# Optimization experiments

Measured on AMD Instinct MI355X. Metric: run time of the kernel, lower is better.

## Reference

```python
import jax, jax.numpy as jnp
import numpy as np

NUM_HEADS = 16
HEAD_DIM = 64
HIDDEN = NUM_HEADS * HEAD_DIM  # 1024
B, S = 4, 2048
SCALE = HEAD_DIM ** -0.5


def setup_inputs() -> dict:
    key = jax.random.key(0)
    ks = jax.random.split(key, 5)
    hidden_states = jax.random.normal(ks[0], (B, S, HIDDEN), dtype=jnp.float32)
    # additive causal mask: 0 on/below diagonal, -1e9 above
    causal = jnp.tril(jnp.ones((S, S), dtype=bool))
    attention_mask = jnp.where(causal, 0.0, -1e9).astype(jnp.float32)[None, None]  # [1,1,S,S]
    init = 1.0 / np.sqrt(HIDDEN)
    wq = jax.random.normal(ks[1], (HIDDEN, HIDDEN), dtype=jnp.float32) * init
    wk = jax.random.normal(ks[2], (HIDDEN, HIDDEN), dtype=jnp.float32) * init
    wv = jax.random.normal(ks[3], (HIDDEN, HIDDEN), dtype=jnp.float32) * init
    wo = jax.random.normal(ks[4], (HIDDEN, HIDDEN), dtype=jnp.float32) * init
    return {"hidden_states": hidden_states, "attention_mask": attention_mask,
            "wq": wq, "wk": wk, "wv": wv, "wo": wo}


def reference(hidden_states, attention_mask, wq, wk, wv, wo):
    b, s, _ = hidden_states.shape
    # nn.Linear(bias=False): y = x @ W^T ; split heads -> [b, h, s, d]
    def proj(w):
        return (hidden_states @ w.T).reshape(b, s, NUM_HEADS, HEAD_DIM).transpose(0, 2, 1, 3)
    q, k, v = proj(wq), proj(wk), proj(wv)
    scores = jnp.einsum('bhqd,bhkd->bhqk', q, k) * SCALE  # [b,h,s,s] materialized
    scores = scores + attention_mask
    probs = jax.nn.softmax(scores, axis=-1)  # dropout is identity (eval / p=0)
    attn = jnp.einsum('bhqk,bhkd->bhqd', probs, v)
    attn = attn.transpose(0, 2, 1, 3).reshape(b, s, HIDDEN)
    return attn @ wo.T
```

## Files before the change

### kernel.cpp

```cpp
#include <hip/hip_runtime.h>

typedef unsigned short u16;
typedef __attribute__((ext_vector_type(8))) short bf16x8;
typedef __attribute__((ext_vector_type(4))) float f32x4;
typedef __attribute__((ext_vector_type(16))) float f32x16;
typedef __attribute__((ext_vector_type(2))) __bf16 bf16x2;

#define NUMH 16
#define HD   64
#define HID  1024
#define BB   4
#define SS   2048
#define MM   (BB*SS)

__device__ __forceinline__ u16 f2bf(float f){
  unsigned u = __builtin_bit_cast(unsigned, f);
  u += 0x7FFFu + ((u >> 16) & 1u);
  return (u16)(u >> 16);
}

__device__ __forceinline__ unsigned pack_bf16(float a, float b){
  bf16x2 t; t[0] = (__bf16)a; t[1] = (__bf16)b;
  return __builtin_bit_cast(unsigned, t);
}

__device__ __forceinline__ float exp2_fast(float x){
  float r; asm("v_exp_f32 %0, %1" : "=v"(r) : "v"(x)); return r;
}

__device__ __forceinline__ void gload_lds16(const void* g, void* l){
  __builtin_amdgcn_global_load_lds((const __attribute__((address_space(1))) void*)g,
                                   (__attribute__((address_space(3))) void*)l, 16, 0, 0);
}

__global__ __launch_bounds__(256) void cast_all(const float* __restrict__ hs,
    const float* __restrict__ wq, const float* __restrict__ wk,
    const float* __restrict__ wv, const float* __restrict__ wo,
    u16* __restrict__ dst)
{
  const int NX4 = MM*HID/4;
  const int NW4 = HID*HID/4;
  int i = blockIdx.x * 256 + threadIdx.x;
  const float* src; int local;
  if (i < NX4){ src = hs; local = i; }
  else {
    int j = i - NX4;
    int wsel = j >> 18;
    local = j & (NW4 - 1);
    src = (wsel == 0) ? wq : ((wsel == 1) ? wk : ((wsel == 2) ? wv : wo));
  }
  float4 v = reinterpret_cast<const float4*>(src)[local];
  ushort4 o = make_ushort4(f2bf(v.x), f2bf(v.y), f2bf(v.z), f2bf(v.w));
  reinterpret_cast<ushort4*>(dst)[i] = o;
}

__global__ __launch_bounds__(256) void gemm_qkv(const u16* __restrict__ A,
    const u16* __restrict__ Wq, const u16* __restrict__ Wk, const u16* __restrict__ Wv,
    u16* __restrict__ Qo, u16* __restrict__ Ko, u16* __restrict__ Vto)
{
  __shared__ alignas(16) u16 As[128*64];
  __shared__ alignas(16) u16 Bs[128*64];
  const int tid = threadIdx.x;
  const int w = tid >> 6, l = tid & 63;
  const int wr = w >> 1, wc = w & 1;
  const int lr = l & 15, lg = l >> 4;
  const int bm = blockIdx.x, bn = blockIdx.y;
  const int which = bn >> 3;
  const int ncol0 = (bn & 7) * 128;
  const u16* __restrict__ Bmat = (which == 0) ? Wq : ((which == 1) ? Wk : Wv);
  const int row0 = bm * 128;

  f32x4 acc[4][4];
  #pragma unroll
  for (int i = 0; i < 4; ++i)
    #pragma unroll
    for (int j = 0; j < 4; ++j)
      acc[i][j] = (f32x4){0.f, 0.f, 0.f, 0.f};

  const int srow = l >> 3;
  const int cg8  = ((l & 7) ^ srow) * 8;

  for (int kt = 0; kt < HID/64; ++kt){
    __syncthreads();
    #pragma unroll
    for (int j = 0; j < 4; ++j){
      int rr = j*32 + w*8 + srow;
      gload_lds16(A    + (size_t)(row0  + rr)*HID + kt*64 + cg8, (char*)As + j*4096 + w*1024);
      gload_lds16(Bmat + (size_t)(ncol0 + rr)*HID + kt*64 + cg8, (char*)Bs + j*4096 + w*1024);
    }
    __syncthreads();
    #pragma unroll
    for (int kk = 0; kk < 2; ++kk){
      bf16x8 af[4], bfr[4];
      #pragma unroll
      for (int i = 0; i < 4; ++i){
        const int offb = ((kk*4 + lg) ^ (lr & 7)) * 16;
        af[i]  = *(const bf16x8*)((const char*)As + (wr*64 + i*16 + lr)*128 + offb);
        bfr[i] = *(const bf16x8*)((const char*)Bs + (wc*64 + i*16 + lr)*128 + offb);
      }
      if (which == 2){
        #pragma unroll
        for (int i = 0; i < 4; ++i)
          #pragma unroll
          for (int j = 0; j < 4; ++j)
            acc[i][j] = __builtin_amdgcn_mfma_f32_16x16x32_bf16(bfr[j], af[i], acc[i][j], 0, 0, 0);
      } else {
        #pragma unroll
        for (int i = 0; i < 4; ++i)
          #pragma unroll
          for (int j = 0; j < 4; ++j)
            acc[i][j] = __builtin_amdgcn_mfma_f32_16x16x32_bf16(af[i], bfr[j], acc[i][j], 0, 0, 0);
      }
    }
  }

  if (which == 2){
    #pragma unroll
    for (int i = 0; i < 4; ++i){
      #pragma unroll
      for (int j = 0; j < 4; ++j){
        #pragma unroll
        for (int r = 0; r < 4; ++r){
          int nl = ncol0 + wc*64 + j*16 + lg*4 + r;
          int gm = row0 + wr*64 + i*16 + lr;
          int b_ = gm >> 11, s = gm & 2047;
          int h  = nl >> 6,  d = nl & 63;
          Vto[(((size_t)b_*NUMH + h)*HD + d)*SS + s] = f2bf(acc[i][j][r]);
        }
      }
    }
  } else {
    #pragma unroll
    for (int i = 0; i < 4; ++i){
      #pragma unroll
      for (int j = 0; j < 4; ++j){
        #pragma unroll
        for (int r = 0; r < 4; ++r){
          int gm = row0 + wr*64 + i*16 + lg*4 + r;
          int nl = ncol0 + wc*64 + j*16 + lr;
          int b_ = gm >> 11, s = gm & 2047;
          int h  = nl >> 6,  d = nl & 63;
          float v = acc[i][j][r];
          if (which == 0)
            Qo[(((size_t)b_*NUMH + h)*SS + s)*HD + d] = f2bf(v * 0.18033688f);
          else
            Ko[(((size_t)b_*NUMH + h)*SS + s)*HD + d] = f2bf(v);
        }
      }
    }
  }
}

__global__ __launch_bounds__(256) void gemm_out(const u16* __restrict__ A,
    const u16* __restrict__ Wo, float* __restrict__ C)
{
  __shared__ alignas(16) u16 As[128*64];
  __shared__ alignas(16) u16 Bs[128*64];
  const int tid = threadIdx.x;
  const int w = tid >> 6, l = tid & 63;
  const int wr = w >> 1, wc = w & 1;
  const int lr = l & 15, lg = l >> 4;
  const int row0 = blockIdx.x * 128;
  const int ncol0 = blockIdx.y * 128;

  f32x4 acc[4][4];
  #pragma unroll
  for (int i = 0; i < 4; ++i)
    #pragma unroll
    for (int j = 0; j < 4; ++j)
      acc[i][j] = (f32x4){0.f, 0.f, 0.f, 0.f};

  const int srow = l >> 3;
  const int cg8  = ((l & 7) ^ srow) * 8;

  for (int kt = 0; kt < HID/64; ++kt){
    __syncthreads();
    #pragma unroll
    for (int j = 0; j < 4; ++j){
      int rr = j*32 + w*8 + srow;
      gload_lds16(A  + (size_t)(row0  + rr)*HID + kt*64 + cg8, (char*)As + j*4096 + w*1024);
      gload_lds16(Wo + (size_t)(ncol0 + rr)*HID + kt*64 + cg8, (char*)Bs + j*4096 + w*1024);
    }
    __syncthreads();
    #pragma unroll
    for (int kk = 0; kk < 2; ++kk){
      bf16x8 af[4], bfr[4];
      #pragma unroll
      for (int i = 0; i < 4; ++i){
        const int offb = ((kk*4 + lg) ^ (lr & 7)) * 16;
        af[i]  = *(const bf16x8*)((const char*)As + (wr*64 + i*16 + lr)*128 + offb);
        bfr[i] = *(const bf16x8*)((const char*)Bs + (wc*64 + i*16 + lr)*128 + offb);
      }
      #pragma unroll
      for (int i = 0; i < 4; ++i)
        #pragma unroll
        for (int j = 0; j < 4; ++j)
          acc[i][j] = __builtin_amdgcn_mfma_f32_16x16x32_bf16(af[i], bfr[j], acc[i][j], 0, 0, 0);
    }
  }

  #pragma unroll
  for (int i = 0; i < 4; ++i)
    #pragma unroll
    for (int j = 0; j < 4; ++j)
      #pragma unroll
      for (int r = 0; r < 4; ++r){
        int gm = row0 + wr*64 + i*16 + lg*4 + r;
        int nl = ncol0 + wc*64 + j*16 + lr;
        C[(size_t)gm*HID + nl] = acc[i][j][r];
      }
}

__device__ __forceinline__ void stage_kv(const u16* __restrict__ Kg, const u16* __restrict__ Vt,
    size_t bhB, int kv0, u16* Kbuf, u16* Vbuf, int w, int l)
{
  #pragma unroll
  for (int i = 0; i < 2; ++i){
    const int r = 32*i + 8*w + (l >> 3);
    const int c16 = (l & 7) ^ (r & 7);
    gload_lds16(Kg + bhB + (size_t)(kv0 + r)*HD + c16*8, (char*)Kbuf + i*4096 + w*1024);
    gload_lds16(Vt + bhB + (size_t)r*SS + kv0 + c16*8,   (char*)Vbuf + i*4096 + w*1024);
  }
}

__global__ __launch_bounds__(256) void attn_fwd(const u16* __restrict__ Qg,
    const u16* __restrict__ Kg, const u16* __restrict__ Vt, u16* __restrict__ AO)
{
  __shared__ alignas(16) u16 Ks[2][64*64];
  __shared__ alignas(16) u16 Vs[2][64*64];

  const int tid = threadIdx.x;
  const int w = tid >> 6, l = tid & 63;
  const int lq = l & 31, hi = l >> 5;
  const int wgid = blockIdx.x;
  const int bh = (wgid & 7) + 8*((wgid >> 3) & 7);
  const int strip = 15 - (wgid >> 6);
  const int b_ = bh >> 4, h = bh & 15;
  const size_t bhB = (size_t)bh * SS * HD;

  const int qs0 = strip * 128;
  const int nt = 2*strip + 2;
  const int q0w = qs0 + 32*w;
  const int qabs = q0w + lq;

  bf16x8 qf[4];
  #pragma unroll
  for (int c = 0; c < 4; ++c)
    qf[c] = *(const bf16x8*)(Qg + bhB + (size_t)qabs*HD + c*16 + hi*8);

  float lsum = 0.f;
  f32x16 oacc[2];
  #pragma unroll
  for (int n = 0; n < 2; ++n)
    #pragma unroll
    for (int r = 0; r < 16; ++r) oacc[n][r] = 0.f;

  int cur = 0;
  stage_kv(Kg, Vt, bhB, 0, Ks[0], Vs[0], w, l);
  __syncthreads();

  for (int t = 0; t < nt; ++t){
    const int kv0 = t*64;
    if (t + 1 < nt)
      stage_kv(Kg, Vt, bhB, (t+1)*64, Ks[cur^1], Vs[cur^1], w, l);

    if (kv0 <= q0w + 31){
      const u16* Kb = Ks[cur];
      const u16* Vb = Vs[cur];
      f32x16 sacc[2];
      #pragma unroll
      for (int mi = 0; mi < 2; ++mi)
        #pragma unroll
        for (int r = 0; r < 16; ++r) sacc[mi][r] = 0.f;
      __builtin_amdgcn_s_setprio(1);
      #pragma unroll
      for (int mi = 0; mi < 2; ++mi){
        const int krow = mi*32 + lq;
        const int sw = (krow & 7) << 4;
        #pragma unroll
        for (int c = 0; c < 4; ++c){
          bf16x8 kf = *(const bf16x8*)((const char*)Kb + krow*128 + ((c*32 + hi*16) ^ sw));
          sacc[mi] = __builtin_amdgcn_mfma_f32_32x32x16_bf16(kf, qf[c], sacc[mi], 0, 0, 0);
        }
      }
      __builtin_amdgcn_s_setprio(0);
      if (kv0 + 63 > q0w){
        #pragma unroll
        for (int mi = 0; mi < 2; ++mi)
          #pragma unroll
          for (int r = 0; r < 16; ++r){
            int kabs = kv0 + mi*32 + (r & 3) + 8*(r >> 2) + 4*hi;
            if (kabs > qabs) sacc[mi][r] = -1e30f;
          }
      }
      float ps[4] = {0.f, 0.f, 0.f, 0.f};
      #pragma unroll
      for (int mi = 0; mi < 2; ++mi)
        #pragma unroll
        for (int r = 0; r < 16; ++r){
          float p = exp2_fast(sacc[mi][r]);
          sacc[mi][r] = p;
          ps[r & 3] += p;
        }
      float psum = (ps[0] + ps[1]) + (ps[2] + ps[3]);
      psum += __shfl_xor(psum, 32);
      lsum += psum;

      bf16x8 pf[4];
      #pragma unroll
      for (int c = 0; c < 4; ++c){
        const int mi = c >> 1;
        const int geb = (c & 1) * 8;
        unsigned a0 = pack_bf16(sacc[mi][geb+0], sacc[mi][geb+1]);
        unsigned a1 = pack_bf16(sacc[mi][geb+2], sacc[mi][geb+3]);
        unsigned b0 = pack_bf16(sacc[mi][geb+4], sacc[mi][geb+5]);
        unsigned b1 = pack_bf16(sacc[mi][geb+6], sacc[mi][geb+7]);
        unsigned sel0 = hi ? b0 : a0, sel1 = hi ? b1 : a1;
        unsigned oth0 = hi ? a0 : b0, oth1 = hi ? a1 : b1;
        unsigned rcv0 = (unsigned)__shfl_xor((int)oth0, 32);
        unsigned rcv1 = (unsigned)__shfl_xor((int)oth1, 32);
        union { unsigned u[4]; bf16x8 v; } pu;
        pu.u[0] = hi ? rcv0 : sel0;
        pu.u[1] = hi ? rcv1 : sel1;
        pu.u[2] = hi ? sel0 : rcv0;
        pu.u[3] = hi ? sel1 : rcv1;
        pf[c] = pu.v;
      }

      __builtin_amdgcn_s_setprio(1);
      #pragma unroll
      for (int n = 0; n < 2; ++n){
        const int drow = n*32 + lq;
        const int swv = (drow & 7) << 4;
        #pragma unroll
        for (int c = 0; c < 4; ++c){
          bf16x8 vf = *(const bf16x8*)((const char*)Vb + drow*128 + ((c*32 + hi*16) ^ swv));
          oacc[n] = __builtin_amdgcn_mfma_f32_32x32x16_bf16(vf, pf[c], oacc[n], 0, 0, 0);
        }
      }
      __builtin_amdgcn_s_setprio(0);
    }
    __syncthreads();
    cur ^= 1;
  }

  const float inv = 1.f / lsum;
  u16* dst = AO + ((size_t)b_*SS + qabs)*HID + h*HD;
  #pragma unroll
  for (int n = 0; n < 2; ++n)
    #pragma unroll
    for (int g = 0; g < 4; ++g){
      ushort4 o;
      o.x = f2bf(oacc[n][4*g+0] * inv);
      o.y = f2bf(oacc[n][4*g+1] * inv);
      o.z = f2bf(oacc[n][4*g+2] * inv);
      o.w = f2bf(oacc[n][4*g+3] * inv);
      *(ushort4*)(dst + n*32 + 8*g + 4*hi) = o;
    }
}

extern "C" void kernel_launch(void* const* d_in, const int* in_sizes, int n_in,
                              void* d_out, int out_size, void* d_ws, size_t ws_size,
                              hipStream_t stream)
{
  const float* hs = (const float*)d_in[0];
  const float* wq = (const float*)d_in[2];
  const float* wk = (const float*)d_in[3];
  const float* wv = (const float*)d_in[4];
  const float* wo = (const float*)d_in[5];

  char* ws = (char*)d_ws;
  u16* Xb  = (u16*)(ws);
  u16* Wqb = (u16*)(ws + ((size_t)16 << 20));
  u16* Wkb = (u16*)(ws + ((size_t)18 << 20));
  u16* Wvb = (u16*)(ws + ((size_t)20 << 20));
  u16* Wob = (u16*)(ws + ((size_t)22 << 20));
  u16* Q   = (u16*)(ws + ((size_t)24 << 20));
  u16* Kb  = (u16*)(ws + ((size_t)40 << 20));
  u16* Vt  = (u16*)(ws + ((size_t)56 << 20));
  u16* AO  = (u16*)(ws + ((size_t)72 << 20));

  cast_all<<<12288, 256, 0, stream>>>(hs, wq, wk, wv, wo, Xb);

  gemm_qkv<<<dim3(64, 24), 256, 0, stream>>>(Xb, Wqb, Wkb, Wvb, Q, Kb, Vt);
  attn_fwd<<<1024, 256, 0, stream>>>(Q, Kb, Vt, AO);
  gemm_out<<<dim3(64, 8), 256, 0, stream>>>(AO, Wob, (float*)d_out);
}
```

Baseline: 154.7 us.

## Triple-buffer QKV GEMM with 256x128 tiles and interleaved async loads

Rewrites the QKV projection GEMM to use 512-thread blocks computing 256x128 tiles, with a three-stage LDS ring in dynamic shared memory (147 KB). Global-to-LDS loads for tile t+2 are issued in pieces between MFMA sub-steps, with explicit vmcnt waits, barriers and setprio around the MFMA clusters. The aim is to hide global load latency and raise arithmetic intensity per block. In exchange it uses far more LDS, halves the grid to 768 blocks, and relies on hand-tuned waitcnt counts that must match the issued loads exactly.

```diff
diff --git a/kernel.cpp b/kernel.cpp
--- a/kernel.cpp
+++ b/kernel.cpp
@@ -54,75 +54,120 @@
   reinterpret_cast<ushort4*>(dst)[i] = o;
 }
 
-__global__ __launch_bounds__(256) void gemm_qkv(const u16* __restrict__ A,
+__global__ __launch_bounds__(512, 2) void gemm_qkv(const u16* __restrict__ A,
     const u16* __restrict__ Wq, const u16* __restrict__ Wk, const u16* __restrict__ Wv,
     u16* __restrict__ Qo, u16* __restrict__ Ko, u16* __restrict__ Vto)
 {
-  __shared__ alignas(16) u16 As[128*64];
-  __shared__ alignas(16) u16 Bs[128*64];
+  extern __shared__ char smem[];
   const int tid = threadIdx.x;
   const int w = tid >> 6, l = tid & 63;
-  const int wr = w >> 1, wc = w & 1;
+  const int wm = w >> 2, wn = w & 3;
   const int lr = l & 15, lg = l >> 4;
   const int bm = blockIdx.x, bn = blockIdx.y;
   const int which = bn >> 3;
   const int ncol0 = (bn & 7) * 128;
   const u16* __restrict__ Bmat = (which == 0) ? Wq : ((which == 1) ? Wk : Wv);
-  const int row0 = bm * 128;
-
-  f32x4 acc[4][4];
-  #pragma unroll
-  for (int i = 0; i < 4; ++i)
-    #pragma unroll
-    for (int j = 0; j < 4; ++j)
-      acc[i][j] = (f32x4){0.f, 0.f, 0.f, 0.f};
-
-  const int srow = l >> 3;
-  const int cg8  = ((l & 7) ^ srow) * 8;
-
-  for (int kt = 0; kt < HID/64; ++kt){
-    __syncthreads();
-    #pragma unroll
-    for (int j = 0; j < 4; ++j){
-      int rr = j*32 + w*8 + srow;
-      gload_lds16(A    + (size_t)(row0  + rr)*HID + kt*64 + cg8, (char*)As + j*4096 + w*1024);
-      gload_lds16(Bmat + (size_t)(ncol0 + rr)*HID + kt*64 + cg8, (char*)Bs + j*4096 + w*1024);
-    }
-    __syncthreads();
-    #pragma unroll
-    for (int kk = 0; kk < 2; ++kk){
-      bf16x8 af[4], bfr[4];
-      #pragma unroll
-      for (int i = 0; i < 4; ++i){
-        const int offb = ((kk*4 + lg) ^ (lr & 7)) * 16;
-        af[i]  = *(const bf16x8*)((const char*)As + (wr*64 + i*16 + lr)*128 + offb);
-        bfr[i] = *(const bf16x8*)((const char*)Bs + (wc*64 + i*16 + lr)*128 + offb);
-      }
+  const int row0 = bm * 256;
+
+  const int sr  = l >> 3;
+  const int cg8 = ((l & 7) ^ sr) * 8;
+  const int dstw = w * 1024;
+
+  auto stageA2 = [&](int kt, int c, int u0){
+    char* base = smem + c * 49152;
+    #pragma unroll
+    for (int u = u0; u < u0 + 2; ++u)
+      gload_lds16(A + (size_t)(row0 + u*64 + w*8 + sr)*HID + kt*64 + cg8,
+                  base + u*8192 + dstw);
+  };
+  auto stageB2 = [&](int kt, int c){
+    char* base = smem + c * 49152 + 32768;
+    #pragma unroll
+    for (int u = 0; u < 2; ++u)
+      gload_lds16(Bmat + (size_t)(ncol0 + u*64 + w*8 + sr)*HID + kt*64 + cg8,
+                  base + u*8192 + dstw);
+  };
+
+  f32x4 acc[8][2] = {};
+
+  stageA2(0, 0, 0); stageA2(0, 0, 2); stageB2(0, 0);
+  stageA2(1, 1, 0); stageA2(1, 1, 2); stageB2(1, 1);
+  asm volatile("s_waitcnt vmcnt(6)" ::: "memory");
+  __builtin_amdgcn_s_barrier();
+  asm volatile("" ::: "memory");
+
+  int c = 0;
+  for (int t = 0; t < 16; ++t){
+    const char* Ab = smem + c * 49152;
+    const char* Bb = Ab + 32768;
+    int c2 = c + 2; if (c2 >= 3) c2 -= 3;
+    const bool pre = (t < 14);
+    bf16x8 bfr[2][2];
+    #pragma unroll
+    for (int p = 0; p < 4; ++p){
+      bf16x8 af[2][2];
+      #pragma unroll
+      for (int i2 = 0; i2 < 2; ++i2){
+        const int row = wm*128 + (2*p + i2)*16 + lr;
+        #pragma unroll
+        for (int kk = 0; kk < 2; ++kk)
+          af[i2][kk] = *(const bf16x8*)(Ab + row*128 + ((kk*4 + lg) ^ (lr & 7))*16);
+      }
+      if (p == 0){
+        #pragma unroll
+        for (int j = 0; j < 2; ++j){
+          const int rowb = wn*32 + j*16 + lr;
+          #pragma unroll
+          for (int kk = 0; kk < 2; ++kk)
+            bfr[j][kk] = *(const bf16x8*)(Bb + rowb*128 + ((kk*4 + lg) ^ (lr & 7))*16);
+        }
+      }
+      if (pre){
+        if (p == 0) stageA2(t+2, c2, 0);
+        else if (p == 1) stageA2(t+2, c2, 2);
+        else if (p == 2) stageB2(t+2, c2);
+      }
+      __builtin_amdgcn_s_barrier();
+      asm volatile("s_waitcnt lgkmcnt(0)" ::: "memory");
+      __builtin_amdgcn_sched_barrier(0);
+      __builtin_amdgcn_s_setprio(1);
       if (which == 2){
         #pragma unroll
-        for (int i = 0; i < 4; ++i)
+        for (int i2 = 0; i2 < 2; ++i2)
           #pragma unroll
-          for (int j = 0; j < 4; ++j)
-            acc[i][j] = __builtin_amdgcn_mfma_f32_16x16x32_bf16(bfr[j], af[i], acc[i][j], 0, 0, 0);
+          for (int j = 0; j < 2; ++j)
+            #pragma unroll
+            for (int kk = 0; kk < 2; ++kk)
+              acc[2*p+i2][j] = __builtin_amdgcn_mfma_f32_16x16x32_bf16(bfr[j][kk], af[i2][kk], acc[2*p+i2][j], 0, 0, 0);
       } else {
         #pragma unroll
-        for (int i = 0; i < 4; ++i)
+        for (int i2 = 0; i2 < 2; ++i2)
           #pragma unroll
-          for (int j = 0; j < 4; ++j)
-            acc[i][j] = __builtin_amdgcn_mfma_f32_16x16x32_bf16(af[i], bfr[j], acc[i][j], 0, 0, 0);
-      }
-    }
+          for (int j = 0; j < 2; ++j)
+            #pragma unroll
+            for (int kk = 0; kk < 2; ++kk)
+              acc[2*p+i2][j] = __builtin_amdgcn_mfma_f32_16x16x32_bf16(af[i2][kk], bfr[j][kk], acc[2*p+i2][j], 0, 0, 0);
+      }
+      __builtin_amdgcn_s_setprio(0);
+      if (p == 3){
+        if (t < 14)       asm volatile("s_waitcnt vmcnt(6)" ::: "memory");
+        else if (t == 14) asm volatile("s_waitcnt vmcnt(0)" ::: "memory");
+      }
+      __builtin_amdgcn_s_barrier();
+      asm volatile("" ::: "memory");
+    }
+    c += 1; if (c == 3) c = 0;
   }
 
   if (which == 2){
     #pragma unroll
-    for (int i = 0; i < 4; ++i){
-      #pragma unroll
-      for (int j = 0; j < 4; ++j){
+    for (int i = 0; i < 8; ++i){
+      #pragma unroll
+      for (int j = 0; j < 2; ++j){
         #pragma unroll
         for (int r = 0; r < 4; ++r){
-          int nl = ncol0 + wc*64 + j*16 + lg*4 + r;
-          int gm = row0 + wr*64 + i*16 + lr;
+          int nl = ncol0 + wn*32 + j*16 + lg*4 + r;
+          int gm = row0 + wm*128 + i*16 + lr;
           int b_ = gm >> 11, s = gm & 2047;
           int h  = nl >> 6,  d = nl & 63;
           Vto[(((size_t)b_*NUMH + h)*HD + d)*SS + s] = f2bf(acc[i][j][r]);
@@ -131,13 +176,13 @@
     }
   } else {
     #pragma unroll
-    for (int i = 0; i < 4; ++i){
-      #pragma unroll
-      for (int j = 0; j < 4; ++j){
+    for (int i = 0; i < 8; ++i){
+      #pragma unroll
+      for (int j = 0; j < 2; ++j){
         #pragma unroll
         for (int r = 0; r < 4; ++r){
-          int gm = row0 + wr*64 + i*16 + lg*4 + r;
-          int nl = ncol0 + wc*64 + j*16 + lr;
+          int gm = row0 + wm*128 + i*16 + lg*4 + r;
+          int nl = ncol0 + wn*32 + j*16 + lr;
           int b_ = gm >> 11, s = gm & 2047;
           int h  = nl >> 6,  d = nl & 63;
           float v = acc[i][j][r];
@@ -380,9 +425,16 @@
   u16* Vt  = (u16*)(ws + ((size_t)56 << 20));
   u16* AO  = (u16*)(ws + ((size_t)72 << 20));
 
+  static int attr_set = 0;
+  if (!attr_set){
+    hipFuncSetAttribute((const void*)gemm_qkv,
+                        hipFuncAttributeMaxDynamicSharedMemorySize, 147456);
+    attr_set = 1;
+  }
+
   cast_all<<<12288, 256, 0, stream>>>(hs, wq, wk, wv, wo, Xb);
 
-  gemm_qkv<<<dim3(64, 24), 256, 0, stream>>>(Xb, Wqb, Wkb, Wvb, Q, Kb, Vt);
+  gemm_qkv<<<dim3(32, 24), 512, 147456, stream>>>(Xb, Wqb, Wkb, Wvb, Q, Kb, Vt);
   attn_fwd<<<1024, 256, 0, stream>>>(Q, Kb, Vt, AO);
   gemm_out<<<dim3(64, 8), 256, 0, stream>>>(AO, Wob, (float*)d_out);
 }
```

New measurement: 166.3 us. +7.5%, slower.

## Triple-buffer QKV GEMM with larger 128x256 tiles and 8-wave blocks

Applied to the files above, without the earlier changes.

The QKV projection GEMM moves from a 128x128 tile with 4 waves and single-buffered LDS to a 128x256 tile with 8 waves. It uses a 3-stage dynamic shared-memory ring (144 KB), so global-to-LDS loads for step t+2 are issued while step t computes. Manual vmcnt waits, barriers and s_setprio around the MFMA block overlap loads with matrix math and reduce the two full syncs per k-step. The cost is much larger LDS use per block, which limits occupancy despite launch_bounds(512,2), and fragile hand-coded wait counts.

```diff
diff --git a/kernel.cpp b/kernel.cpp
--- a/kernel.cpp
+++ b/kernel.cpp
@@ -54,50 +54,71 @@
   reinterpret_cast<ushort4*>(dst)[i] = o;
 }
 
-__global__ __launch_bounds__(256) void gemm_qkv(const u16* __restrict__ A,
+__global__ __launch_bounds__(512, 2) void gemm_qkv(const u16* __restrict__ A,
     const u16* __restrict__ Wq, const u16* __restrict__ Wk, const u16* __restrict__ Wv,
     u16* __restrict__ Qo, u16* __restrict__ Ko, u16* __restrict__ Vto)
 {
-  __shared__ alignas(16) u16 As[128*64];
-  __shared__ alignas(16) u16 Bs[128*64];
+  extern __shared__ char smem[];
   const int tid = threadIdx.x;
   const int w = tid >> 6, l = tid & 63;
-  const int wr = w >> 1, wc = w & 1;
+  const int wm = w >> 2, wn = w & 3;
   const int lr = l & 15, lg = l >> 4;
   const int bm = blockIdx.x, bn = blockIdx.y;
-  const int which = bn >> 3;
-  const int ncol0 = (bn & 7) * 128;
+  const int which = bn >> 2;
+  const int ncol0 = (bn & 3) * 256;
   const u16* __restrict__ Bmat = (which == 0) ? Wq : ((which == 1) ? Wk : Wv);
   const int row0 = bm * 128;
 
-  f32x4 acc[4][4];
-  #pragma unroll
-  for (int i = 0; i < 4; ++i)
-    #pragma unroll
-    for (int j = 0; j < 4; ++j)
-      acc[i][j] = (f32x4){0.f, 0.f, 0.f, 0.f};
-
-  const int srow = l >> 3;
-  const int cg8  = ((l & 7) ^ srow) * 8;
-
-  for (int kt = 0; kt < HID/64; ++kt){
-    __syncthreads();
-    #pragma unroll
-    for (int j = 0; j < 4; ++j){
-      int rr = j*32 + w*8 + srow;
-      gload_lds16(A    + (size_t)(row0  + rr)*HID + kt*64 + cg8, (char*)As + j*4096 + w*1024);
-      gload_lds16(Bmat + (size_t)(ncol0 + rr)*HID + kt*64 + cg8, (char*)Bs + j*4096 + w*1024);
-    }
-    __syncthreads();
+  const int sr  = l >> 3;
+  const int cg8 = ((l & 7) ^ sr) * 8;
+  const int dstw = w * 1024;
+
+  auto stageA = [&](int kt, int c){
+    char* base = smem + c * 49152;
+    #pragma unroll
+    for (int u = 0; u < 2; ++u)
+      gload_lds16(A + (size_t)(row0 + u*64 + w*8 + sr)*HID + kt*64 + cg8,
+                  base + u*8192 + dstw);
+  };
+  auto stageB = [&](int kt, int c, int u0, int n){
+    char* base = smem + c * 49152 + 16384;
+    for (int u = u0; u < u0 + n; ++u)
+      gload_lds16(Bmat + (size_t)(ncol0 + u*64 + w*8 + sr)*HID + kt*64 + cg8,
+                  base + u*8192 + dstw);
+  };
+
+  f32x4 acc[4][4] = {};
+
+  stageA(0, 0); stageB(0, 0, 0, 4);
+  stageA(1, 1); stageB(1, 1, 0, 4);
+  asm volatile("s_waitcnt vmcnt(6)" ::: "memory");
+  __builtin_amdgcn_s_barrier();
+  asm volatile("" ::: "memory");
+
+  int c = 0;
+  for (int t = 0; t < 16; ++t){
+    const char* Ab = smem + c * 49152;
+    const char* Bb = Ab + 16384;
+    int c2 = c + 2; if (c2 >= 3) c2 -= 3;
+    const bool pre = (t < 14);
     #pragma unroll
     for (int kk = 0; kk < 2; ++kk){
       bf16x8 af[4], bfr[4];
-      #pragma unroll
-      for (int i = 0; i < 4; ++i){
-        const int offb = ((kk*4 + lg) ^ (lr & 7)) * 16;
-        af[i]  = *(const bf16x8*)((const char*)As + (wr*64 + i*16 + lr)*128 + offb);
-        bfr[i] = *(const bf16x8*)((const char*)Bs + (wc*64 + i*16 + lr)*128 + offb);
-      }
+      const int offb = ((kk*4 + lg) ^ (lr & 7)) * 16;
+      #pragma unroll
+      for (int i = 0; i < 4; ++i)
+        af[i]  = *(const bf16x8*)(Ab + (wm*64 + i*16 + lr)*128 + offb);
+      #pragma unroll
+      for (int j = 0; j < 4; ++j)
+        bfr[j] = *(const bf16x8*)(Bb + (wn*64 + j*16 + lr)*128 + offb);
+      if (pre){
+        if (kk == 0){ stageA(t+2, c2); stageB(t+2, c2, 0, 1); }
+        else        { stageB(t+2, c2, 1, 3); }
+      }
+      __builtin_amdgcn_s_barrier();
+      asm volatile("s_waitcnt lgkmcnt(0)" ::: "memory");
+      __builtin_amdgcn_sched_barrier(0);
+      __builtin_amdgcn_s_setprio(1);
       if (which == 2){
         #pragma unroll
         for (int i = 0; i < 4; ++i)
@@ -111,7 +132,15 @@
           for (int j = 0; j < 4; ++j)
             acc[i][j] = __builtin_amdgcn_mfma_f32_16x16x32_bf16(af[i], bfr[j], acc[i][j], 0, 0, 0);
       }
-    }
+      __builtin_amdgcn_s_setprio(0);
+      if (kk == 1){
+        if (t < 14)       asm volatile("s_waitcnt vmcnt(6)" ::: "memory");
+        else if (t == 14) asm volatile("s_waitcnt vmcnt(0)" ::: "memory");
+      }
+      __builtin_amdgcn_s_barrier();
+      asm volatile("" ::: "memory");
+    }
+    c += 1; if (c == 3) c = 0;
   }
 
   if (which == 2){
@@ -121,8 +150,8 @@
       for (int j = 0; j < 4; ++j){
         #pragma unroll
         for (int r = 0; r < 4; ++r){
-          int nl = ncol0 + wc*64 + j*16 + lg*4 + r;
-          int gm = row0 + wr*64 + i*16 + lr;
+          int nl = ncol0 + wn*64 + j*16 + lg*4 + r;
+          int gm = row0 + wm*64 + i*16 + lr;
           int b_ = gm >> 11, s = gm & 2047;
           int h  = nl >> 6,  d = nl & 63;
           Vto[(((size_t)b_*NUMH + h)*HD + d)*SS + s] = f2bf(acc[i][j][r]);
@@ -136,8 +165,8 @@
       for (int j = 0; j < 4; ++j){
         #pragma unroll
         for (int r = 0; r < 4; ++r){
-          int gm = row0 + wr*64 + i*16 + lg*4 + r;
-          int nl = ncol0 + wc*64 + j*16 + lr;
+          int gm = row0 + wm*64 + i*16 + lg*4 + r;
+          int nl = ncol0 + wn*64 + j*16 + lr;
           int b_ = gm >> 11, s = gm & 2047;
           int h  = nl >> 6,  d = nl & 63;
           float v = acc[i][j][r];
@@ -380,9 +409,16 @@
   u16* Vt  = (u16*)(ws + ((size_t)56 << 20));
   u16* AO  = (u16*)(ws + ((size_t)72 << 20));
 
+  static int attr_set = 0;
+  if (!attr_set){
+    hipFuncSetAttribute((const void*)gemm_qkv,
+                        hipFuncAttributeMaxDynamicSharedMemorySize, 147456);
+    attr_set = 1;
+  }
+
   cast_all<<<12288, 256, 0, stream>>>(hs, wq, wk, wv, wo, Xb);
 
-  gemm_qkv<<<dim3(64, 24), 256, 0, stream>>>(Xb, Wqb, Wkb, Wvb, Q, Kb, Vt);
+  gemm_qkv<<<dim3(64, 12), 512, 147456, stream>>>(Xb, Wqb, Wkb, Wvb, Q, Kb, Vt);
   attn_fwd<<<1024, 256, 0, stream>>>(Q, Kb, Vt, AO);
   gemm_out<<<dim3(64, 8), 256, 0, stream>>>(AO, Wob, (float*)d_out);
 }
```

Measured after the change: 155.8 us. About the same (+0.7%).

## Read K/V fragments directly from global memory instead of LDS double-buffering

Applied to the files above, without the earlier changes.

The attention kernel no longer stages K and V tiles into double-buffered shared memory with async global-to-LDS loads and block-wide barriers. Each wave now loads its MFMA operand fragments straight from global memory and loops only up to its own causal limit. This removes barrier synchronisation and LDS traffic, and lets waves with fewer tiles finish early. In exchange each wave re-fetches K/V from global/L2 (four times the global traffic per block), loses the prefetch overlap, and does strided uncoalesced V reads.

```diff
diff --git a/kernel.cpp b/kernel.cpp
--- a/kernel.cpp
+++ b/kernel.cpp
@@ -211,24 +211,9 @@
       }
 }
 
-__device__ __forceinline__ void stage_kv(const u16* __restrict__ Kg, const u16* __restrict__ Vt,
-    size_t bhB, int kv0, u16* Kbuf, u16* Vbuf, int w, int l)
-{
-  #pragma unroll
-  for (int i = 0; i < 2; ++i){
-    const int r = 32*i + 8*w + (l >> 3);
-    const int c16 = (l & 7) ^ (r & 7);
-    gload_lds16(Kg + bhB + (size_t)(kv0 + r)*HD + c16*8, (char*)Kbuf + i*4096 + w*1024);
-    gload_lds16(Vt + bhB + (size_t)r*SS + kv0 + c16*8,   (char*)Vbuf + i*4096 + w*1024);
-  }
-}
-
 __global__ __launch_bounds__(256) void attn_fwd(const u16* __restrict__ Qg,
     const u16* __restrict__ Kg, const u16* __restrict__ Vt, u16* __restrict__ AO)
 {
-  __shared__ alignas(16) u16 Ks[2][64*64];
-  __shared__ alignas(16) u16 Vs[2][64*64];
-
   const int tid = threadIdx.x;
   const int w = tid >> 6, l = tid & 63;
   const int lq = l & 31, hi = l >> 5;
@@ -239,9 +224,12 @@
   const size_t bhB = (size_t)bh * SS * HD;
 
   const int qs0 = strip * 128;
-  const int nt = 2*strip + 2;
   const int q0w = qs0 + 32*w;
   const int qabs = q0w + lq;
+  const int tmax = (q0w + 31) >> 6;
+
+  const u16* __restrict__ Kbase = Kg + bhB;
+  const u16* __restrict__ Vbase = Vt + bhB;
 
   bf16x8 qf[4];
   #pragma unroll
@@ -255,93 +243,78 @@
     #pragma unroll
     for (int r = 0; r < 16; ++r) oacc[n][r] = 0.f;
 
-  int cur = 0;
-  stage_kv(Kg, Vt, bhB, 0, Ks[0], Vs[0], w, l);
-  __syncthreads();
-
-  for (int t = 0; t < nt; ++t){
+  for (int t = 0; t <= tmax; ++t){
     const int kv0 = t*64;
-    if (t + 1 < nt)
-      stage_kv(Kg, Vt, bhB, (t+1)*64, Ks[cur^1], Vs[cur^1], w, l);
-
-    if (kv0 <= q0w + 31){
-      const u16* Kb = Ks[cur];
-      const u16* Vb = Vs[cur];
-      f32x16 sacc[2];
+    f32x16 sacc[2];
+    #pragma unroll
+    for (int mi = 0; mi < 2; ++mi)
+      #pragma unroll
+      for (int r = 0; r < 16; ++r) sacc[mi][r] = 0.f;
+    __builtin_amdgcn_s_setprio(1);
+    #pragma unroll
+    for (int mi = 0; mi < 2; ++mi){
+      const int krow = mi*32 + lq;
+      #pragma unroll
+      for (int c = 0; c < 4; ++c){
+        bf16x8 kf = *(const bf16x8*)(Kbase + (size_t)(kv0 + krow)*HD + c*16 + hi*8);
+        sacc[mi] = __builtin_amdgcn_mfma_f32_32x32x16_bf16(kf, qf[c], sacc[mi], 0, 0, 0);
+      }
+    }
+    __builtin_amdgcn_s_setprio(0);
+    if (kv0 + 63 > q0w){
       #pragma unroll
       for (int mi = 0; mi < 2; ++mi)
         #pragma unroll
-        for (int r = 0; r < 16; ++r) sacc[mi][r] = 0.f;
-      __builtin_amdgcn_s_setprio(1);
-      #pragma unroll
-      for (int mi = 0; mi < 2; ++mi){
-        const int krow = mi*32 + lq;
-        const int sw = (krow & 7) << 4;
-        #pragma unroll
-        for (int c = 0; c < 4; ++c){
-          bf16x8 kf = *(const bf16x8*)((const char*)Kb + krow*128 + ((c*32 + hi*16) ^ sw));
-          sacc[mi] = __builtin_amdgcn_mfma_f32_32x32x16_bf16(kf, qf[c], sacc[mi], 0, 0, 0);
+        for (int r = 0; r < 16; ++r){
+          int kabs = kv0 + mi*32 + (r & 3) + 8*(r >> 2) + 4*hi;
+          if (kabs > qabs) sacc[mi][r] = -1e30f;
         }
-      }
-      __builtin_amdgcn_s_setprio(0);
-      if (kv0 + 63 > q0w){
-        #pragma unroll
-        for (int mi = 0; mi < 2; ++mi)
-          #pragma unroll
-          for (int r = 0; r < 16; ++r){
-            int kabs = kv0 + mi*32 + (r & 3) + 8*(r >> 2) + 4*hi;
-            if (kabs > qabs) sacc[mi][r] = -1e30f;
-          }
-      }
-      float ps[4] = {0.f, 0.f, 0.f, 0.f};
-      #pragma unroll
-      for (int mi = 0; mi < 2; ++mi)
-        #pragma unroll
-        for (int r = 0; r < 16; ++r){
-          float p = exp2_fast(sacc[mi][r]);
-          sacc[mi][r] = p;
-          ps[r & 3] += p;
-        }
-      float psum = (ps[0] + ps[1]) + (ps[2] + ps[3]);
-      psum += __shfl_xor(psum, 32);
-      lsum += psum;
-
-      bf16x8 pf[4];
+    }
+    float ps[4] = {0.f, 0.f, 0.f, 0.f};
+    #pragma unroll
+    for (int mi = 0; mi < 2; ++mi)
+      #pragma unroll
+      for (int r = 0; r < 16; ++r){
+        float p = exp2_fast(sacc[mi][r]);
+        sacc[mi][r] = p;
+        ps[r & 3] += p;
+      }
+    float psum = (ps[0] + ps[1]) + (ps[2] + ps[3]);
+    psum += __shfl_xor(psum, 32);
+    lsum += psum;
+
+    bf16x8 pf[4];
+    #pragma unroll
+    for (int c = 0; c < 4; ++c){
+      const int mi = c >> 1;
+      const int geb = (c & 1) * 8;
+      unsigned a0 = pack_bf16(sacc[mi][geb+0], sacc[mi][geb+1]);
+      unsigned a1 = pack_bf16(sacc[mi][geb+2], sacc[mi][geb+3]);
+      unsigned b0 = pack_bf16(sacc[mi][geb+4], sacc[mi][geb+5]);
+      unsigned b1 = pack_bf16(sacc[mi][geb+6], sacc[mi][geb+7]);
+      unsigned sel0 = hi ? b0 : a0, sel1 = hi ? b1 : a1;
+      unsigned oth0 = hi ? a0 : b0, oth1 = hi ? a1 : b1;
+      unsigned rcv0 = (unsigned)__shfl_xor((int)oth0, 32);
+      unsigned rcv1 = (unsigned)__shfl_xor((int)oth1, 32);
+      union { unsigned u[4]; bf16x8 v; } pu;
+      pu.u[0] = hi ? rcv0 : sel0;
+      pu.u[1] = hi ? rcv1 : sel1;
+      pu.u[2] = hi ? sel0 : rcv0;
+      pu.u[3] = hi ? sel1 : rcv1;
+      pf[c] = pu.v;
+    }
+
+    __builtin_amdgcn_s_setprio(1);
+    #pragma unroll
+    for (int n = 0; n < 2; ++n){
+      const int drow = n*32 + lq;
       #pragma unroll
       for (int c = 0; c < 4; ++c){
-        const int mi = c >> 1;
-        const int geb = (c & 1) * 8;
-        unsigned a0 = pack_bf16(sacc[mi][geb+0], sacc[mi][geb+1]);
-        unsigned a1 = pack_bf16(sacc[mi][geb+2], sacc[mi][geb+3]);
-        unsigned b0 = pack_bf16(sacc[mi][geb+4], sacc[mi][geb+5]);
-        unsigned b1 = pack_bf16(sacc[mi][geb+6], sacc[mi][geb+7]);
-        unsigned sel0 = hi ? b0 : a0, sel1 = hi ? b1 : a1;
-        unsigned oth0 = hi ? a0 : b0, oth1 = hi ? a1 : b1;
-        unsigned rcv0 = (unsigned)__shfl_xor((int)oth0, 32);
-        unsigned rcv1 = (unsigned)__shfl_xor((int)oth1, 32);
-        union { unsigned u[4]; bf16x8 v; } pu;
-        pu.u[0] = hi ? rcv0 : sel0;
-        pu.u[1] = hi ? rcv1 : sel1;
-        pu.u[2] = hi ? sel0 : rcv0;
-        pu.u[3] = hi ? sel1 : rcv1;
-        pf[c] = pu.v;
-      }
-
-      __builtin_amdgcn_s_setprio(1);
-      #pragma unroll
-      for (int n = 0; n < 2; ++n){
-        const int drow = n*32 + lq;
-        const int swv = (drow & 7) << 4;
-        #pragma unroll
-        for (int c = 0; c < 4; ++c){
-          bf16x8 vf = *(const bf16x8*)((const char*)Vb + drow*128 + ((c*32 + hi*16) ^ swv));
-          oacc[n] = __builtin_amdgcn_mfma_f32_32x32x16_bf16(vf, pf[c], oacc[n], 0, 0, 0);
-        }
-      }
-      __builtin_amdgcn_s_setprio(0);
-    }
-    __syncthreads();
-    cur ^= 1;
+        bf16x8 vf = *(const bf16x8*)(Vbase + (size_t)drow*SS + kv0 + c*16 + hi*8);
+        oacc[n] = __builtin_amdgcn_mfma_f32_32x32x16_bf16(vf, pf[c], oacc[n], 0, 0, 0);
+      }
+    }
+    __builtin_amdgcn_s_setprio(0);
   }
 
   const float inv = 1.f / lsum;
```

Result: slower. 230.5 us (+49.0%).
